# Kernel tuning notes

Measured on AMD Instinct MI355X. Metric: run time of the kernel, lower is better.

Reference implementation:

```python
import jax, jax.numpy as jnp
import numpy as np

N, M, K, C, FF, H, OUT = 20000, 80000, 48, 64, 256, 4, 64


def _lin(x, w, b):
    return x @ w.T + b


def _bn(x, g, b, eps=1e-5):
    mu = x.mean(0)
    var = x.var(0)
    return (x - mu) * jax.lax.rsqrt(var + eps) * g + b


def setup_inputs() -> dict:
    key = jax.random.key(0)
    ks = jax.random.split(key, 24)
    voxel_features = jax.random.normal(ks[0], (M, C), jnp.float32)
    voxel_coords = jax.random.normal(ks[1], (M, 3), jnp.float32)
    query_coords = jax.random.normal(ks[2], (N, 3), jnp.float32)
    idx = jax.random.randint(ks[3], (N, K), 0, M)
    drop = jax.random.uniform(ks[4], (N, K)) < 0.1
    drop = drop.at[:, 0].set(False)  # keep >=1 valid key per query
    key_indices = jnp.where(drop, -1, idx)
    s = 0.05
    p = lambda i, shp: jax.random.normal(ks[i], shp, jnp.float32) * s
    return {
        "voxel_features": voxel_features,
        "voxel_coords": voxel_coords,
        "query_coords": query_coords,
        "key_indices": key_indices,
        "q_w": p(5, (C, 3)), "q_b": p(6, (C,)),
        "kpos_w": p(7, (C, 3)), "kpos_b": p(8, (C,)),
        "in_w": p(9, (3 * C, C)), "in_b": p(10, (3 * C,)),
        "out_w": p(11, (C, C)), "out_b": p(12, (C,)),
        "lin1_w": p(13, (FF, C)), "lin1_b": p(14, (FF,)),
        "lin2_w": p(15, (C, FF)), "lin2_b": p(16, (C,)),
        "norm_g": jnp.ones((C,), jnp.float32), "norm_b": jnp.zeros((C,), jnp.float32),
        "outl_w": p(17, (OUT, C)), "outl_b": p(18, (OUT,)),
        "obn_g": jnp.ones((OUT,), jnp.float32), "obn_b": jnp.zeros((OUT,), jnp.float32),
    }


def reference(voxel_features, voxel_coords, query_coords, key_indices,
              q_w, q_b, kpos_w, kpos_b, in_w, in_b, out_w, out_b,
              lin1_w, lin1_b, lin2_w, lin2_b, norm_g, norm_b,
              outl_w, outl_b, obn_g, obn_b):
    hd = C // H
    mask = key_indices < 0                      # (N,K) padded keys
    safe = jnp.where(mask, 0, key_indices)
    key_feats = voxel_features[safe]            # (N,K,C) hash-gather
    key_coords = voxel_coords[safe]             # (N,K,3)
    # query positional projection
    q_feat = jax.nn.relu(_lin(query_coords, q_w, q_b))          # (N,C)
    # relative coords + key positional conv1d(kernel=1) == linear on coord dim
    rel = key_coords - query_coords[:, None, :]                  # (N,K,3)
    key_feats = key_feats + jax.nn.relu(_lin(rel, kpos_w, kpos_b))
    # multihead attention, query length 1 per voxel
    Wq, Wk, Wv = jnp.split(in_w, 3, axis=0)
    bq, bk, bv = jnp.split(in_b, 3)
    q = (_lin(q_feat, Wq, bq) / jnp.sqrt(jnp.float32(hd))).reshape(N, H, hd)
    k = _lin(key_feats, Wk, bk).reshape(N, K, H, hd)
    v = _lin(key_feats, Wv, bv).reshape(N, K, H, hd)
    scores = jnp.einsum('nhd,nkhd->nhk', q, k)
    scores = jnp.where(mask[:, None, :], -jnp.inf, scores)
    attn = jax.nn.softmax(scores, axis=-1)
    ctx = jnp.einsum('nhk,nkhd->nhd', attn, v).reshape(N, C)
    att = _lin(ctx, out_w, out_b)                                # (N,C)
    # FFN + residual
    x = att + _lin(jax.nn.relu(_lin(att, lin1_w, lin1_b)), lin2_w, lin2_b)
    x = _bn(x, norm_g, norm_b)
    # output layer: Linear -> BN -> ReLU
    x = jax.nn.relu(_bn(_lin(x, outl_w, outl_b), obn_g, obn_b))
    return x
```

## Files before the change

### kernel.cpp

```cpp
#include <hip/hip_runtime.h>
#include <math.h>

#define N_Q 20000
#define KK 48
#define CC 64
#define FFD 256

#define TW_WOT   0
#define TW_WVT   4096
#define TW_L1B   8192
#define TW_L2B   16384
#define TW_OLB   24576
#define TW_QB    26624
#define TW_KB    28672
#define ST_OFF   32768
#define M_OFF    33024
#define VF_OFF   2593024

typedef short bf16x8 __attribute__((ext_vector_type(8)));
typedef float f32x4  __attribute__((ext_vector_type(4)));

__device__ __forceinline__ unsigned f2bf(float f) {
    unsigned u = __float_as_uint(f);
    return (u + 0x7fffu + ((u >> 16) & 1u)) >> 16;
}
__device__ __forceinline__ unsigned pk2(float a, float b) {
    return f2bf(a) | (f2bf(b) << 16);
}
__device__ __forceinline__ float bflo(unsigned u) { return __uint_as_float(u << 16); }
__device__ __forceinline__ float bfhi(unsigned u) { return __uint_as_float(u & 0xffff0000u); }
__device__ __forceinline__ bf16x8 ldfrag(const unsigned short* p) {
    return *(const bf16x8*)p;
}

__global__ void prep_all(const float* __restrict__ in_w,
                         const float* __restrict__ out_w,
                         const float* __restrict__ lin1_w,
                         const float* __restrict__ lin2_w,
                         const float* __restrict__ outl_w,
                         const float* __restrict__ vfeat,
                         float* __restrict__ tw,
                         unsigned short* __restrict__ vfeat_bf,
                         float* __restrict__ stats)
{
    int t = blockIdx.x * 256 + threadIdx.x;
    unsigned* twu = (unsigned*)tw;
    if (t < 1280000) {
        float4 v = ((const float4*)vfeat)[t];
        uint2 p; p.x = pk2(v.x, v.y); p.y = pk2(v.z, v.w);
        ((uint2*)vfeat_bf)[t] = p;
    }
    if (t < 256) stats[t] = 0.0f;
    if (t < 4096) {
        int c = t >> 6, j = t & 63;
        tw[TW_WOT + j*64 + c] = out_w[c*64 + j];
    } else if (t < 8192) {
        int i = t - 4096, cp = i >> 6, c = i & 63;
        tw[TW_WVT + cp*64 + c] = in_w[(128 + c)*64 + cp];
    } else if (t < 16384) {
        int p = t - 8192;
        int j2 = p & 3, lane = (p >> 2) & 63, nb = (p >> 8) & 15, ks = p >> 12;
        int n = nb*16 + (lane & 15), k = ks*32 + (lane >> 4)*8 + 2*j2;
        twu[TW_L1B + p] = pk2(lin1_w[n*64 + k], lin1_w[n*64 + k + 1]);
    } else if (t < 24576) {
        int p = t - 16384;
        int j2 = p & 3, lane = (p >> 2) & 63, nb = (p >> 8) & 3, ks = p >> 10;
        int n = nb*16 + (lane & 15), k = ks*32 + (lane >> 4)*8 + 2*j2;
        twu[TW_L2B + p] = pk2(lin2_w[n*256 + k], lin2_w[n*256 + k + 1]);
    } else if (t < 26624) {
        int p = t - 24576;
        int j2 = p & 3, lane = (p >> 2) & 63, nb = (p >> 8) & 3, ks = p >> 10;
        int n = nb*16 + (lane & 15), k = ks*32 + (lane >> 4)*8 + 2*j2;
        twu[TW_OLB + p] = pk2(outl_w[n*64 + k], outl_w[n*64 + k + 1]);
    } else if (t < 28672) {
        int p = t - 26624;
        int j2 = p & 3, lane = (p >> 2) & 63, nb = (p >> 8) & 3, ks = p >> 10;
        int n = nb*16 + (lane & 15), k = ks*32 + (lane >> 4)*8 + 2*j2;
        twu[TW_QB + p] = pk2(in_w[n*64 + k], in_w[n*64 + k + 1]);
    } else if (t < 32768) {
        int p = t - 28672;
        int j2 = p & 3, lane = (p >> 2) & 63, nb = (p >> 8) & 3, h = p >> 10;
        int j = nb*16 + (lane & 15), k = (lane >> 4)*8 + 2*j2;
        unsigned u = 0;
        if (k < 16)
            u = pk2(in_w[(64 + h*16 + k)*64 + j], in_w[(64 + h*16 + k + 1)*64 + j]);
        twu[TW_KB + p] = u;
    }
}

__global__ __launch_bounds__(256) void m_kernel(
    const float* __restrict__ qcoord, const float* __restrict__ q_w,
    const float* __restrict__ q_b, const float* __restrict__ in_b,
    const float* __restrict__ tw, unsigned short* __restrict__ M_all)
{
    __shared__ __align__(16) unsigned short sQF[80*72];
    __shared__ __align__(16) unsigned short sQ[80*72];
    int t = threadIdx.x, base = blockIdx.x * 80;
    int colq = (t*4) & 63;
    float qwv[12];
    #pragma unroll
    for (int j = 0; j < 12; ++j) qwv[j] = q_w[colq*3 + j];
    float4 qb4 = *(const float4*)&q_b[colq];
    #pragma unroll
    for (int i = 0; i < 5; ++i) {
        int e = i*1024 + t*4, r = e >> 6, n = base + r;
        float c0 = qcoord[n*3], c1 = qcoord[n*3+1], c2 = qcoord[n*3+2];
        float f0 = fmaxf(fmaf(qwv[2],  c2, fmaf(qwv[1],  c1, fmaf(qwv[0], c0, qb4.x))), 0.f);
        float f1 = fmaxf(fmaf(qwv[5],  c2, fmaf(qwv[4],  c1, fmaf(qwv[3], c0, qb4.y))), 0.f);
        float f2 = fmaxf(fmaf(qwv[8],  c2, fmaf(qwv[7],  c1, fmaf(qwv[6], c0, qb4.z))), 0.f);
        float f3 = fmaxf(fmaf(qwv[11], c2, fmaf(qwv[10], c1, fmaf(qwv[9], c0, qb4.w))), 0.f);
        uint2 p; p.x = pk2(f0, f1); p.y = pk2(f2, f3);
        *(uint2*)&sQF[r*72 + colq] = p;
    }
    int w = t >> 6, lane = t & 63, l16 = lane & 15, quad = lane >> 4;
    const unsigned* QB = (const unsigned*)(tw + TW_QB);
    const unsigned* KB = (const unsigned*)(tw + TW_KB);
    bf16x8 qbf[2], kbf[4];
    #pragma unroll
    for (int ks = 0; ks < 2; ++ks)
        qbf[ks] = ldfrag((const unsigned short*)&QB[((ks*4 + w)*64 + lane)*4]);
    #pragma unroll
    for (int nb = 0; nb < 4; ++nb)
        kbf[nb] = ldfrag((const unsigned short*)&KB[((w*4 + nb)*64 + lane)*4]);
    __syncthreads();

    int cq = w*16 + l16;
    float bq = in_b[cq];
    #pragma unroll
    for (int mb = 0; mb < 5; ++mb) {
        bf16x8 a0 = ldfrag(&sQF[(mb*16 + l16)*72 + quad*8]);
        bf16x8 a1 = ldfrag(&sQF[(mb*16 + l16)*72 + 32 + quad*8]);
        f32x4 acc = {0.f, 0.f, 0.f, 0.f};
        acc = __builtin_amdgcn_mfma_f32_16x16x32_bf16(a0, qbf[0], acc, 0, 0, 0);
        acc = __builtin_amdgcn_mfma_f32_16x16x32_bf16(a1, qbf[1], acc, 0, 0, 0);
        #pragma unroll
        for (int reg = 0; reg < 4; ++reg) {
            int row = mb*16 + quad*4 + reg;
            sQ[row*72 + cq] = (unsigned short)f2bf((acc[reg] + bq) * 0.25f);
        }
    }
    #pragma unroll
    for (int mb = 0; mb < 5; ++mb) {
        bf16x8 a = {0,0,0,0,0,0,0,0};
        if (quad < 2) a = ldfrag(&sQ[(mb*16 + l16)*72 + w*16 + quad*8]);
        f32x4 acc[4];
        #pragma unroll
        for (int nb = 0; nb < 4; ++nb) {
            f32x4 z = {0.f, 0.f, 0.f, 0.f};
            acc[nb] = __builtin_amdgcn_mfma_f32_16x16x32_bf16(a, kbf[nb], z, 0, 0, 0);
        }
        #pragma unroll
        for (int nb = 0; nb < 4; ++nb)
            #pragma unroll
            for (int reg = 0; reg < 4; ++reg) {
                int r = base + mb*16 + quad*4 + reg, j = nb*16 + l16;
                M_all[(size_t)r*256 + j*4 + w] = (unsigned short)f2bf(acc[nb][reg]);
            }
    }
}

__global__ __launch_bounds__(64, 4) void attn_kernel(
    const unsigned short* __restrict__ vfeat_bf, const float* __restrict__ vcoord,
    const float* __restrict__ qcoord, const int* __restrict__ kidx,
    const float* __restrict__ kpos_w, const float* __restrict__ kpos_b,
    const float* __restrict__ in_b, const float* __restrict__ out_b,
    const float* __restrict__ tw, const unsigned short* __restrict__ M_all,
    float* __restrict__ att_out)
{
    __shared__ __align__(16) unsigned short skf[KK*72];
    __shared__ __align__(16) float reg1[256];
    int n = blockIdx.x, c = threadIdx.x;
    int l16 = c & 15, h = c >> 4;
    float* sM   = reg1;
    float* sP   = reg1;
    float* sctx = reg1 + 192;
    float* sT   = (float*)skf;

    {
        uint2 mu = ((const uint2*)(M_all + (size_t)n*256))[c];
        float4 mf;
        mf.x = bflo(mu.x); mf.y = bfhi(mu.x);
        mf.z = bflo(mu.y); mf.w = bfhi(mu.y);
        *(float4*)&sM[4*c] = mf;
    }

    float qc0 = qcoord[n*3+0], qc1 = qcoord[n*3+1], qc2 = qcoord[n*3+2];

    int kread = c < 48 ? c : 47;
    int idxv = kidx[(size_t)n*KK + kread];
    int sfe = idxv < 0 ? 0 : idxv;
    float rl0 = vcoord[sfe*3+0] - qc0;
    float rl1 = vcoord[sfe*3+1] - qc1;
    float rl2 = vcoord[sfe*3+2] - qc2;

    float4 wA  = *(const float4*)(kpos_w + 12*l16 + 0);
    float4 wB  = *(const float4*)(kpos_w + 12*l16 + 4);
    float4 wC  = *(const float4*)(kpos_w + 12*l16 + 8);
    float4 kb4 = *(const float4*)(kpos_b + 4*l16);

    uint2 fv[12];
    #pragma unroll
    for (int i = 0; i < 12; ++i) {
        int row = 4*i + h;
        int si = __shfl(idxv, row);
        si = si < 0 ? 0 : si;
        fv[i] = *(const uint2*)(vfeat_bf + (size_t)si*64 + 4*l16);
    }
    #pragma unroll
    for (int i = 0; i < 12; ++i) {
        int row = 4*i + h;
        float rr0 = __shfl(rl0, row), rr1 = __shfl(rl1, row), rr2 = __shfl(rl2, row);
        float g0 = bflo(fv[i].x), g1 = bfhi(fv[i].x);
        float g2 = bflo(fv[i].y), g3 = bfhi(fv[i].y);
        g0 += fmaxf(fmaf(wA.x, rr0, fmaf(wA.y, rr1, fmaf(wA.z, rr2, kb4.x))), 0.0f);
        g1 += fmaxf(fmaf(wA.w, rr0, fmaf(wB.x, rr1, fmaf(wB.y, rr2, kb4.y))), 0.0f);
        g2 += fmaxf(fmaf(wB.z, rr0, fmaf(wB.w, rr1, fmaf(wC.x, rr2, kb4.z))), 0.0f);
        g3 += fmaxf(fmaf(wC.y, rr0, fmaf(wC.z, rr1, fmaf(wC.w, rr2, kb4.w))), 0.0f);
        uint2 p; p.x = pk2(g0, g1); p.y = pk2(g2, g3);
        *(uint2*)&skf[row*72 + 4*l16] = p;
    }

    int i0 = __shfl(idxv, l16), i1 = __shfl(idxv, l16 + 16), i2 = __shfl(idxv, l16 + 32);
    float S0 = 0, S1 = 0, S2 = 0;
    #pragma unroll
    for (int j8 = 0; j8 < 8; ++j8) {
        uint2 A = *(const uint2*)&skf[ l16       *72 + 8*j8];
        uint2 A2= *(const uint2*)&skf[ l16       *72 + 8*j8 + 4];
        uint2 B = *(const uint2*)&skf[(l16 + 16) *72 + 8*j8];
        uint2 B2= *(const uint2*)&skf[(l16 + 16) *72 + 8*j8 + 4];
        uint2 D = *(const uint2*)&skf[(l16 + 32) *72 + 8*j8];
        uint2 D2= *(const uint2*)&skf[(l16 + 32) *72 + 8*j8 + 4];
        #pragma unroll
        for (int jj = 0; jj < 8; ++jj) {
            unsigned ua = (jj < 4) ? ((jj < 2) ? A.x : A.y) : ((jj < 6) ? A2.x : A2.y);
            unsigned ub = (jj < 4) ? ((jj < 2) ? B.x : B.y) : ((jj < 6) ? B2.x : B2.y);
            unsigned ud = (jj < 4) ? ((jj < 2) ? D.x : D.y) : ((jj < 6) ? D2.x : D2.y);
            float av = (jj & 1) ? bfhi(ua) : bflo(ua);
            float bv = (jj & 1) ? bfhi(ub) : bflo(ub);
            float dv = (jj & 1) ? bfhi(ud) : bflo(ud);
            float m  = sM[(8*j8 + jj)*4 + h];
            S0 = fmaf(av, m, S0);
            S1 = fmaf(bv, m, S1);
            S2 = fmaf(dv, m, S2);
        }
    }
    if (i0 < 0) S0 = -INFINITY;
    if (i1 < 0) S1 = -INFINITY;
    if (i2 < 0) S2 = -INFINITY;

    float mx = fmaxf(S0, fmaxf(S1, S2));
    #pragma unroll
    for (int off = 8; off >= 1; off >>= 1) mx = fmaxf(mx, __shfl_xor(mx, off, 16));
    float e0 = __expf(S0 - mx), e1 = __expf(S1 - mx), e2 = __expf(S2 - mx);
    float es = e0 + e1 + e2;
    #pragma unroll
    for (int off = 8; off >= 1; off >>= 1) es += __shfl_xor(es, off, 16);
    float rinv = 1.0f / es;
    sP[ l16       *4 + h] = e0 * rinv;
    sP[(l16 + 16) *4 + h] = e1 * rinv;
    sP[(l16 + 32) *4 + h] = e2 * rinv;

    float T0 = 0, T1 = 0, T2 = 0, T3 = 0;
    #pragma unroll 8
    for (int k = 0; k < KK; ++k) {
        float kf = __uint_as_float(((unsigned)skf[k*72 + c]) << 16);
        float4 p = *(const float4*)&sP[k*4];
        T0 = fmaf(p.x, kf, T0); T1 = fmaf(p.y, kf, T1);
        T2 = fmaf(p.z, kf, T2); T3 = fmaf(p.w, kf, T3);
    }
    sT[0*65 + c] = T0; sT[1*65 + c] = T1; sT[2*65 + c] = T2; sT[3*65 + c] = T3;

    const float* WvT = tw + TW_WVT;
    float ctx = in_b[128 + c];
    #pragma unroll 8
    for (int cp = 0; cp < 64; ++cp)
        ctx = fmaf(sT[h*65 + cp], WvT[cp*64 + c], ctx);
    sctx[c] = ctx;

    const float* WoT = tw + TW_WOT;
    float att = out_b[c];
    #pragma unroll 8
    for (int j = 0; j < 64; ++j)
        att = fmaf(sctx[j], WoT[j*64 + c], att);
    att_out[(size_t)n*64 + c] = att;
}

__global__ __launch_bounds__(256) void ffn_kernel(
    const float* __restrict__ tw, const float* __restrict__ lin1_b,
    const float* __restrict__ lin2_b, float* __restrict__ att_y,
    float* __restrict__ sum1, float* __restrict__ sumsq1)
{
    __shared__ __align__(16) unsigned short sA[80*72];
    __shared__ __align__(16) unsigned short sH[80*264];
    int t = threadIdx.x, base = blockIdx.x * 80;
    #pragma unroll
    for (int i = 0; i < 5; ++i) {
        int e = i*1024 + t*4, r = e >> 6, col = e & 63;
        float4 v = *(const float4*)&att_y[(size_t)(base + r)*64 + col];
        uint2 p; p.x = pk2(v.x, v.y); p.y = pk2(v.z, v.w);
        *(uint2*)&sA[r*72 + col] = p;
    }
    int w = t >> 6, lane = t & 63, l16 = lane & 15, quad = lane >> 4;
    const unsigned* L1B = (const unsigned*)(tw + TW_L1B);
    const unsigned* L2B = (const unsigned*)(tw + TW_L2B);
    bf16x8 b1f[2][4], b2f[8];
    #pragma unroll
    for (int ks = 0; ks < 2; ++ks)
        #pragma unroll
        for (int nb = 0; nb < 4; ++nb)
            b1f[ks][nb] = ldfrag((const unsigned short*)&L1B[((ks*16 + w*4 + nb)*64 + lane)*4]);
    #pragma unroll
    for (int ks = 0; ks < 8; ++ks)
        b2f[ks] = ldfrag((const unsigned short*)&L2B[((ks*4 + w)*64 + lane)*4]);
    __syncthreads();

    #pragma unroll
    for (int mb = 0; mb < 5; ++mb) {
        bf16x8 a0 = ldfrag(&sA[(mb*16 + l16)*72 + quad*8]);
        bf16x8 a1 = ldfrag(&sA[(mb*16 + l16)*72 + 32 + quad*8]);
        #pragma unroll
        for (int nb = 0; nb < 4; ++nb) {
            f32x4 acc = {0.f, 0.f, 0.f, 0.f};
            acc = __builtin_amdgcn_mfma_f32_16x16x32_bf16(a0, b1f[0][nb], acc, 0, 0, 0);
            acc = __builtin_amdgcn_mfma_f32_16x16x32_bf16(a1, b1f[1][nb], acc, 0, 0, 0);
            int f = w*64 + nb*16 + l16;
            float bias = lin1_b[f];
            #pragma unroll
            for (int reg = 0; reg < 4; ++reg) {
                int row = mb*16 + quad*4 + reg;
                sH[row*264 + f] = (unsigned short)f2bf(fmaxf(acc[reg] + bias, 0.0f));
            }
        }
    }
    __syncthreads();

    int c = w*16 + l16;
    float lb2 = lin2_b[c];
    float s = 0.f, ss = 0.f;
    #pragma unroll
    for (int mb = 0; mb < 5; ++mb) {
        f32x4 acc = {0.f, 0.f, 0.f, 0.f};
        #pragma unroll
        for (int ks = 0; ks < 8; ++ks) {
            bf16x8 a = ldfrag(&sH[(mb*16 + l16)*264 + ks*32 + quad*8]);
            acc = __builtin_amdgcn_mfma_f32_16x16x32_bf16(a, b2f[ks], acc, 0, 0, 0);
        }
        #pragma unroll
        for (int reg = 0; reg < 4; ++reg) {
            int r = base + mb*16 + quad*4 + reg;
            float y = att_y[(size_t)r*64 + c] + lb2 + acc[reg];
            att_y[(size_t)r*64 + c] = y;
            s += y; ss = fmaf(y, y, ss);
        }
    }
    s  += __shfl_xor(s, 16);  s  += __shfl_xor(s, 32);
    ss += __shfl_xor(ss, 16); ss += __shfl_xor(ss, 32);
    if (lane < 16) {
        atomicAdd(&sum1[c], s);
        atomicAdd(&sumsq1[c], ss);
    }
}

__global__ __launch_bounds__(256) void linout_kernel(
    const float* __restrict__ tw, const float* __restrict__ outl_b,
    const float* __restrict__ norm_g, const float* __restrict__ norm_b,
    const float* __restrict__ sum1, const float* __restrict__ sumsq1,
    const float* __restrict__ y, float* __restrict__ z_out,
    float* __restrict__ sum2, float* __restrict__ sumsq2)
{
    __shared__ __align__(16) unsigned short sX[80*72];
    int t = threadIdx.x, base = blockIdx.x * 80;
    int colq = (t*4) & 63;
    const float invN = 1.0f / 20000.0f;
    float4 sm = *(const float4*)&sum1[colq];
    float4 sq = *(const float4*)&sumsq1[colq];
    float4 g  = *(const float4*)&norm_g[colq];
    float4 bb = *(const float4*)&norm_b[colq];
    float mu0 = sm.x*invN, mu1 = sm.y*invN, mu2 = sm.z*invN, mu3 = sm.w*invN;
    float a0 = g.x / sqrtf(fmaf(-mu0, mu0, sq.x*invN) + 1e-5f);
    float a1 = g.y / sqrtf(fmaf(-mu1, mu1, sq.y*invN) + 1e-5f);
    float a2 = g.z / sqrtf(fmaf(-mu2, mu2, sq.z*invN) + 1e-5f);
    float a3 = g.w / sqrtf(fmaf(-mu3, mu3, sq.w*invN) + 1e-5f);
    float b0 = fmaf(-mu0, a0, bb.x), b1 = fmaf(-mu1, a1, bb.y);
    float b2 = fmaf(-mu2, a2, bb.z), b3 = fmaf(-mu3, a3, bb.w);
    #pragma unroll
    for (int i = 0; i < 5; ++i) {
        int e = i*1024 + t*4, r = e >> 6;
        float4 v = *(const float4*)&y[(size_t)(base + r)*64 + colq];
        uint2 p;
        p.x = pk2(fmaf(v.x, a0, b0), fmaf(v.y, a1, b1));
        p.y = pk2(fmaf(v.z, a2, b2), fmaf(v.w, a3, b3));
        *(uint2*)&sX[r*72 + colq] = p;
    }
    int w = t >> 6, lane = t & 63, l16 = lane & 15, quad = lane >> 4;
    const unsigned* OLB = (const unsigned*)(tw + TW_OLB);
    bf16x8 obf[2];
    #pragma unroll
    for (int ks = 0; ks < 2; ++ks)
        obf[ks] = ldfrag((const unsigned short*)&OLB[((ks*4 + w)*64 + lane)*4]);
    __syncthreads();

    int co = w*16 + l16;
    float ob = outl_b[co];
    float s = 0.f, ss = 0.f;
    #pragma unroll
    for (int mb = 0; mb < 5; ++mb) {
        bf16x8 x0 = ldfrag(&sX[(mb*16 + l16)*72 + quad*8]);
        bf16x8 x1 = ldfrag(&sX[(mb*16 + l16)*72 + 32 + quad*8]);
        f32x4 acc = {0.f, 0.f, 0.f, 0.f};
        acc = __builtin_amdgcn_mfma_f32_16x16x32_bf16(x0, obf[0], acc, 0, 0, 0);
        acc = __builtin_amdgcn_mfma_f32_16x16x32_bf16(x1, obf[1], acc, 0, 0, 0);
        #pragma unroll
        for (int reg = 0; reg < 4; ++reg) {
            int r = base + mb*16 + quad*4 + reg;
            float zv = acc[reg] + ob;
            z_out[(size_t)r*64 + co] = zv;
            s += zv; ss = fmaf(zv, zv, ss);
        }
    }
    s  += __shfl_xor(s, 16);  s  += __shfl_xor(s, 32);
    ss += __shfl_xor(ss, 16); ss += __shfl_xor(ss, 32);
    if (lane < 16) {
        atomicAdd(&sum2[co], s);
        atomicAdd(&sumsq2[co], ss);
    }
}

__global__ void final_kernel(float* __restrict__ z,
    const float* __restrict__ sum2, const float* __restrict__ sumsq2,
    const float* __restrict__ obn_g, const float* __restrict__ obn_b)
{
    int i = blockIdx.x*blockDim.x + threadIdx.x;
    if (i >= N_Q*64/4) return;
    int o4 = (i*4) & 63;
    float4 sm = *(const float4*)&sum2[o4];
    float4 sq = *(const float4*)&sumsq2[o4];
    float4 g  = *(const float4*)&obn_g[o4];
    float4 b  = *(const float4*)&obn_b[o4];
    const float invN = 1.0f / 20000.0f;
    float mux = sm.x*invN, muy = sm.y*invN, muz = sm.z*invN, muw = sm.w*invN;
    float ax = g.x / sqrtf(fmaf(-mux, mux, sq.x*invN) + 1e-5f);
    float ay = g.y / sqrtf(fmaf(-muy, muy, sq.y*invN) + 1e-5f);
    float az = g.z / sqrtf(fmaf(-muz, muz, sq.z*invN) + 1e-5f);
    float aw = g.w / sqrtf(fmaf(-muw, muw, sq.w*invN) + 1e-5f);
    float4 v = ((float4*)z)[i];
    v.x = fmaxf(fmaf(v.x - mux, ax, b.x), 0.0f);
    v.y = fmaxf(fmaf(v.y - muy, ay, b.y), 0.0f);
    v.z = fmaxf(fmaf(v.z - muz, az, b.z), 0.0f);
    v.w = fmaxf(fmaf(v.w - muw, aw, b.w), 0.0f);
    ((float4*)z)[i] = v;
}

extern "C" void kernel_launch(void* const* d_in, const int* in_sizes, int n_in,
                              void* d_out, int out_size, void* d_ws, size_t ws_size,
                              hipStream_t stream)
{
    const float* vfeat  = (const float*)d_in[0];
    const float* vcoord = (const float*)d_in[1];
    const float* qcoord = (const float*)d_in[2];
    const int*   kidx   = (const int*)d_in[3];
    const float* q_w    = (const float*)d_in[4];
    const float* q_b    = (const float*)d_in[5];
    const float* kpos_w = (const float*)d_in[6];
    const float* kpos_b = (const float*)d_in[7];
    const float* in_w   = (const float*)d_in[8];
    const float* in_b   = (const float*)d_in[9];
    const float* out_w  = (const float*)d_in[10];
    const float* out_b  = (const float*)d_in[11];
    const float* lin1_w = (const float*)d_in[12];
    const float* lin1_b = (const float*)d_in[13];
    const float* lin2_w = (const float*)d_in[14];
    const float* lin2_b = (const float*)d_in[15];
    const float* norm_g = (const float*)d_in[16];
    const float* norm_b = (const float*)d_in[17];
    const float* outl_w = (const float*)d_in[18];
    const float* outl_b = (const float*)d_in[19];
    const float* obn_g  = (const float*)d_in[20];
    const float* obn_b  = (const float*)d_in[21];

    float* ws = (float*)d_ws;
    float* tw = ws;
    float* stats = ws + ST_OFF;
    float* sum1 = stats, *sumsq1 = stats + 64, *sum2 = stats + 128, *sumsq2 = stats + 192;
    unsigned short* M_all = (unsigned short*)(ws + M_OFF);
    unsigned short* vfeat_bf = (unsigned short*)(ws + VF_OFF);
    float* xd = (float*)d_out;

    prep_all<<<5120, 256, 0, stream>>>(in_w, out_w, lin1_w, lin2_w, outl_w,
                                       vfeat, tw, vfeat_bf, stats);
    m_kernel<<<250, 256, 0, stream>>>(qcoord, q_w, q_b, in_b, tw, M_all);
    attn_kernel<<<N_Q, 64, 0, stream>>>(vfeat_bf, vcoord, qcoord, kidx, kpos_w, kpos_b,
                                        in_b, out_b, tw, M_all, xd);
    ffn_kernel<<<250, 256, 0, stream>>>(tw, lin1_b, lin2_b, xd, sum1, sumsq1);
    linout_kernel<<<250, 256, 0, stream>>>(tw, outl_b, norm_g, norm_b, sum1, sumsq1,
                                           xd, xd, sum2, sumsq2);
    final_kernel<<<1250, 256, 0, stream>>>(xd, sum2, sumsq2, obn_g, obn_b);
}
```

Baseline: 199.2 us.

## Move attention scores and value projection in attn_kernel onto MFMA

Computes attention scores with bf16 MFMA against the per-query M vectors, whose layout changes to head-major, and computes the V projection per key with MFMA before weighting by the softmax probabilities. This replaces the scalar FMA loops and the LDS staging of scores, probabilities and the intermediate T. Wv is now pre-packed into bf16 MFMA fragment layout. The cost is extra V-projection work per key (48x64x64) instead of per head after the probability reduction, plus many cross-lane shuffles and lower-precision bf16 weights.

```diff
diff --git a/kernel.cpp b/kernel.cpp
--- a/kernel.cpp
+++ b/kernel.cpp
@@ -55,8 +55,12 @@
         int c = t >> 6, j = t & 63;
         tw[TW_WOT + j*64 + c] = out_w[c*64 + j];
     } else if (t < 8192) {
-        int i = t - 4096, cp = i >> 6, c = i & 63;
-        tw[TW_WVT + cp*64 + c] = in_w[(128 + c)*64 + cp];
+        if (t < 6144) {
+            int p = t - 4096;
+            int j2 = p & 3, lane = (p >> 2) & 63, nb = (p >> 8) & 3, ks = p >> 10;
+            int nn = nb*16 + (lane & 15), k = ks*32 + (lane >> 4)*8 + 2*j2;
+            twu[TW_WVT + p] = pk2(in_w[(128 + nn)*64 + k], in_w[(128 + nn)*64 + k + 1]);
+        }
     } else if (t < 16384) {
         int p = t - 8192;
         int j2 = p & 3, lane = (p >> 2) & 63, nb = (p >> 8) & 15, ks = p >> 12;
@@ -154,7 +158,7 @@
             #pragma unroll
             for (int reg = 0; reg < 4; ++reg) {
                 int r = base + mb*16 + quad*4 + reg, j = nb*16 + l16;
-                M_all[(size_t)r*256 + j*4 + w] = (unsigned short)f2bf(acc[nb][reg]);
+                M_all[(size_t)r*256 + w*64 + j] = (unsigned short)f2bf(acc[nb][reg]);
             }
     }
 }
@@ -168,21 +172,20 @@
     float* __restrict__ att_out)
 {
     __shared__ __align__(16) unsigned short skf[KK*72];
-    __shared__ __align__(16) float reg1[256];
+    __shared__ __align__(16) float sctx[64];
     int n = blockIdx.x, c = threadIdx.x;
-    int l16 = c & 15, h = c >> 4;
-    float* sM   = reg1;
-    float* sP   = reg1;
-    float* sctx = reg1 + 192;
-    float* sT   = (float*)skf;
-
-    {
-        uint2 mu = ((const uint2*)(M_all + (size_t)n*256))[c];
-        float4 mf;
-        mf.x = bflo(mu.x); mf.y = bfhi(mu.x);
-        mf.z = bflo(mu.y); mf.w = bfhi(mu.y);
-        *(float4*)&sM[4*c] = mf;
-    }
+    int l16 = c & 15, quad = c >> 4;
+
+    const unsigned short* Mrow = M_all + (size_t)n*256 + (l16 & 3)*64 + quad*8;
+    bf16x8 mf0 = ldfrag(Mrow);
+    bf16x8 mf1 = ldfrag(Mrow + 32);
+    const unsigned* VBu = (const unsigned*)(tw + TW_WVT);
+    bf16x8 wv[2][4];
+    #pragma unroll
+    for (int ks = 0; ks < 2; ++ks)
+        #pragma unroll
+        for (int nb = 0; nb < 4; ++nb)
+            wv[ks][nb] = ldfrag((const unsigned short*)&VBu[((ks*4 + nb)*64 + c)*4]);
 
     float qc0 = qcoord[n*3+0], qc1 = qcoord[n*3+1], qc2 = qcoord[n*3+2];
 
@@ -201,14 +204,14 @@
     uint2 fv[12];
     #pragma unroll
     for (int i = 0; i < 12; ++i) {
-        int row = 4*i + h;
+        int row = 4*i + quad;
         int si = __shfl(idxv, row);
         si = si < 0 ? 0 : si;
         fv[i] = *(const uint2*)(vfeat_bf + (size_t)si*64 + 4*l16);
     }
     #pragma unroll
     for (int i = 0; i < 12; ++i) {
-        int row = 4*i + h;
+        int row = 4*i + quad;
         float rr0 = __shfl(rl0, row), rr1 = __shfl(rl1, row), rr2 = __shfl(rl2, row);
         float g0 = bflo(fv[i].x), g1 = bfhi(fv[i].x);
         float g2 = bflo(fv[i].y), g3 = bfhi(fv[i].y);
@@ -220,62 +223,73 @@
         *(uint2*)&skf[row*72 + 4*l16] = p;
     }
 
-    int i0 = __shfl(idxv, l16), i1 = __shfl(idxv, l16 + 16), i2 = __shfl(idxv, l16 + 32);
-    float S0 = 0, S1 = 0, S2 = 0;
-    #pragma unroll
-    for (int j8 = 0; j8 < 8; ++j8) {
-        uint2 A = *(const uint2*)&skf[ l16       *72 + 8*j8];
-        uint2 A2= *(const uint2*)&skf[ l16       *72 + 8*j8 + 4];
-        uint2 B = *(const uint2*)&skf[(l16 + 16) *72 + 8*j8];
-        uint2 B2= *(const uint2*)&skf[(l16 + 16) *72 + 8*j8 + 4];
-        uint2 D = *(const uint2*)&skf[(l16 + 32) *72 + 8*j8];
-        uint2 D2= *(const uint2*)&skf[(l16 + 32) *72 + 8*j8 + 4];
-        #pragma unroll
-        for (int jj = 0; jj < 8; ++jj) {
-            unsigned ua = (jj < 4) ? ((jj < 2) ? A.x : A.y) : ((jj < 6) ? A2.x : A2.y);
-            unsigned ub = (jj < 4) ? ((jj < 2) ? B.x : B.y) : ((jj < 6) ? B2.x : B2.y);
-            unsigned ud = (jj < 4) ? ((jj < 2) ? D.x : D.y) : ((jj < 6) ? D2.x : D2.y);
-            float av = (jj & 1) ? bfhi(ua) : bflo(ua);
-            float bv = (jj & 1) ? bfhi(ub) : bflo(ub);
-            float dv = (jj & 1) ? bfhi(ud) : bflo(ud);
-            float m  = sM[(8*j8 + jj)*4 + h];
-            S0 = fmaf(av, m, S0);
-            S1 = fmaf(bv, m, S1);
-            S2 = fmaf(dv, m, S2);
-        }
-    }
-    if (i0 < 0) S0 = -INFINITY;
-    if (i1 < 0) S1 = -INFINITY;
-    if (i2 < 0) S2 = -INFINITY;
-
-    float mx = fmaxf(S0, fmaxf(S1, S2));
-    #pragma unroll
-    for (int off = 8; off >= 1; off >>= 1) mx = fmaxf(mx, __shfl_xor(mx, off, 16));
-    float e0 = __expf(S0 - mx), e1 = __expf(S1 - mx), e2 = __expf(S2 - mx);
-    float es = e0 + e1 + e2;
-    #pragma unroll
-    for (int off = 8; off >= 1; off >>= 1) es += __shfl_xor(es, off, 16);
+    unsigned long long vm = __ballot(c < 48 && idxv >= 0);
+    bf16x8 a0s[3], a1s[3];
+    float S[3][4];
+    #pragma unroll
+    for (int mb = 0; mb < 3; ++mb) {
+        a0s[mb] = ldfrag(&skf[(mb*16 + l16)*72 + quad*8]);
+        a1s[mb] = ldfrag(&skf[(mb*16 + l16)*72 + 32 + quad*8]);
+        f32x4 acc = {0.f, 0.f, 0.f, 0.f};
+        acc = __builtin_amdgcn_mfma_f32_16x16x32_bf16(a0s[mb], mf0, acc, 0, 0, 0);
+        acc = __builtin_amdgcn_mfma_f32_16x16x32_bf16(a1s[mb], mf1, acc, 0, 0, 0);
+        #pragma unroll
+        for (int r = 0; r < 4; ++r) {
+            int kk = mb*16 + quad*4 + r;
+            S[mb][r] = ((vm >> kk) & 1ull) ? acc[r] : -1e30f;
+        }
+    }
+
+    float mx = S[0][0];
+    #pragma unroll
+    for (int mb = 0; mb < 3; ++mb)
+        #pragma unroll
+        for (int r = 0; r < 4; ++r) mx = fmaxf(mx, S[mb][r]);
+    mx = fmaxf(mx, __shfl_xor(mx, 16));
+    mx = fmaxf(mx, __shfl_xor(mx, 32));
+    float p[3][4], es = 0.f;
+    #pragma unroll
+    for (int mb = 0; mb < 3; ++mb)
+        #pragma unroll
+        for (int r = 0; r < 4; ++r) { p[mb][r] = __expf(S[mb][r] - mx); es += p[mb][r]; }
+    es += __shfl_xor(es, 16);
+    es += __shfl_xor(es, 32);
     float rinv = 1.0f / es;
-    sP[ l16       *4 + h] = e0 * rinv;
-    sP[(l16 + 16) *4 + h] = e1 * rinv;
-    sP[(l16 + 32) *4 + h] = e2 * rinv;
-
-    float T0 = 0, T1 = 0, T2 = 0, T3 = 0;
-    #pragma unroll 8
-    for (int k = 0; k < KK; ++k) {
-        float kf = __uint_as_float(((unsigned)skf[k*72 + c]) << 16);
-        float4 p = *(const float4*)&sP[k*4];
-        T0 = fmaf(p.x, kf, T0); T1 = fmaf(p.y, kf, T1);
-        T2 = fmaf(p.z, kf, T2); T3 = fmaf(p.w, kf, T3);
-    }
-    sT[0*65 + c] = T0; sT[1*65 + c] = T1; sT[2*65 + c] = T2; sT[3*65 + c] = T3;
-
-    const float* WvT = tw + TW_WVT;
-    float ctx = in_b[128 + c];
-    #pragma unroll 8
-    for (int cp = 0; cp < 64; ++cp)
-        ctx = fmaf(sT[h*65 + cp], WvT[cp*64 + c], ctx);
-    sctx[c] = ctx;
+    #pragma unroll
+    for (int mb = 0; mb < 3; ++mb)
+        #pragma unroll
+        for (int r = 0; r < 4; ++r) p[mb][r] *= rinv;
+
+    float cacc0 = 0.f, cacc1 = 0.f, cacc2 = 0.f, cacc3 = 0.f;
+    #pragma unroll
+    for (int mb = 0; mb < 3; ++mb) {
+        f32x4 av[4];
+        #pragma unroll
+        for (int nb = 0; nb < 4; ++nb) {
+            f32x4 z = {0.f, 0.f, 0.f, 0.f};
+            z = __builtin_amdgcn_mfma_f32_16x16x32_bf16(a0s[mb], wv[0][nb], z, 0, 0, 0);
+            av[nb] = __builtin_amdgcn_mfma_f32_16x16x32_bf16(a1s[mb], wv[1][nb], z, 0, 0, 0);
+        }
+        #pragma unroll
+        for (int r = 0; r < 4; ++r) {
+            float pv = p[mb][r];
+            float p0 = __shfl(pv, quad*16 + 0);
+            float p1 = __shfl(pv, quad*16 + 1);
+            float p2 = __shfl(pv, quad*16 + 2);
+            float p3 = __shfl(pv, quad*16 + 3);
+            cacc0 = fmaf(p0, av[0][r], cacc0);
+            cacc1 = fmaf(p1, av[1][r], cacc1);
+            cacc2 = fmaf(p2, av[2][r], cacc2);
+            cacc3 = fmaf(p3, av[3][r], cacc3);
+        }
+    }
+    cacc0 += __shfl_xor(cacc0, 16); cacc0 += __shfl_xor(cacc0, 32);
+    cacc1 += __shfl_xor(cacc1, 16); cacc1 += __shfl_xor(cacc1, 32);
+    cacc2 += __shfl_xor(cacc2, 16); cacc2 += __shfl_xor(cacc2, 32);
+    cacc3 += __shfl_xor(cacc3, 16); cacc3 += __shfl_xor(cacc3, 32);
+    float cv = quad == 0 ? cacc0 : quad == 1 ? cacc1 : quad == 2 ? cacc2 : cacc3;
+    cv += in_b[128 + c];
+    sctx[c] = cv;
 
     const float* WoT = tw + TW_WOT;
     float att = out_b[c];
```

Result: faster. 185.6 us (-6.8%).
